# Kernel tuning notes

Hardware: AMD Instinct MI355X
Metric: run time of the kernel (lower is better)

The kernel has to match this reference:

```python
import jax, jax.numpy as jnp
import numpy as np
import math

NFFT = 2048; HOP = 512; BINS = NFFT // 2 + 1  # 1025
HEADS = 2; D = 2 * BINS; DFF = 4 * D          # 2050, 8200
BATCH = 4; LEN = 441000


def _stft(x, window):
    # replicates torch.stft(center=True, pad_mode='reflect', onesided=True)
    pad = NFFT // 2
    xp = jnp.pad(x, ((0, 0), (pad, pad)), mode='reflect')
    n_frames = 1 + (xp.shape[-1] - NFFT) // HOP
    idx = jnp.arange(n_frames)[:, None] * HOP + jnp.arange(NFFT)[None, :]
    frames = xp[:, idx] * window                      # (N, T, NFFT)
    return jnp.fft.rfft(frames, axis=-1).transpose(0, 2, 1)  # (N, BINS, T)


def _istft(spec, window, length):
    # replicates torch.istft(center=True, length=length)
    frames = jnp.fft.irfft(spec.transpose(0, 2, 1), n=NFFT, axis=-1) * window  # (N,T,NFFT)
    T = frames.shape[1]
    out_len = NFFT + HOP * (T - 1)
    idx = jnp.arange(T)[:, None] * HOP + jnp.arange(NFFT)[None, :]
    out = jnp.zeros((frames.shape[0], out_len), frames.dtype).at[:, idx].add(frames)
    wsq = jnp.zeros((out_len,), window.dtype).at[idx].add(window ** 2)
    out = out / jnp.where(wsq > 1e-11, wsq, 1.0)
    pad = NFFT // 2
    return out[:, pad:pad + length]


def _pos_enc(d, T):
    pos = jnp.arange(T, dtype=jnp.float32)[:, None]
    div = jnp.exp(jnp.arange(0, d, 2, dtype=jnp.float32) * (-math.log(10000.0) / d))
    pe = jnp.zeros((T, d), jnp.float32)
    pe = pe.at[:, 0::2].set(jnp.sin(pos * div)).at[:, 1::2].set(jnp.cos(pos * div))
    return pe[None]


def _ln(x, g, b):
    m = x.mean(-1, keepdims=True)
    v = x.var(-1, keepdims=True)
    return (x - m) / jnp.sqrt(v + 1e-5) * g + b


def _clin(r, i, Wr, br, Wi, bi):
    # (Lr(r) - Li(i), Lr(i) + Li(r))
    return (r @ Wr.T + br) - (i @ Wi.T + bi), (i @ Wr.T + br) + (r @ Wi.T + bi)


def _cconv1x1(r, i, wr, br, wi, bi):
    # 1x1 grouped conv with in=out=2, groups=2 -> per-channel scale+bias
    s = lambda x, w, b: x * w[None, :, None, None] + b[None, :, None, None]
    return s(r, wr, br) - s(i, wi, bi), s(i, wr, br) + s(r, wi, bi)


def _cattn(r, i, Win, bin_, Wo, bo):
    # 8 shared-weight MHA calls; only 4 distinct (Q,K) softmax maps, each
    # applied to two V tensors (the fusion opportunity). Eval mode: no dropout.
    B, S, _ = r.shape
    hd = D // HEADS
    Wq, Wk, Wv = Win[:D], Win[D:2 * D], Win[2 * D:]
    bq, bk, bv = bin_[:D], bin_[D:2 * D], bin_[2 * D:]
    proj = lambda x, W, b: (x @ W.T + b).reshape(B, S, HEADS, hd).transpose(0, 2, 1, 3)
    qr, qi = proj(r, Wq, bq), proj(i, Wq, bq)
    kr, ki = proj(r, Wk, bk), proj(i, Wk, bk)
    vr, vi = proj(r, Wv, bv), proj(i, Wv, bv)
    scale = 1.0 / math.sqrt(hd)
    A = lambda q, k: jax.nn.softmax(jnp.einsum('bhqd,bhkd->bhqk', q, k) * scale, axis=-1)
    Arr, Ari, Air, Aii = A(qr, kr), A(qr, ki), A(qi, kr), A(qi, ki)
    ap = lambda Aw, v: jnp.einsum('bhqk,bhkd->bhqd', Aw, v)
    out_r = ap(Arr, vr) + ap(Ari, vi) - ap(Air, vi) - ap(Aii, vr)
    out_i = ap(Arr, vi) + ap(Ari, vr) + ap(Air, vr) - ap(Aii, vi)
    merge = lambda o: o.transpose(0, 2, 1, 3).reshape(B, S, D)
    # out_proj bias coefficients: real part (+1+1-1-1)=0, imag part (+1+1+1-1)=2
    return merge(out_r) @ Wo.T, merge(out_i) @ Wo.T + 2.0 * bo


def reference(mix, window, c1wr, c1br, c1wi, c1bi, c2wr, c2br, c2wi, c2bi,
              attn_in_w, attn_in_b, attn_out_w, attn_out_b,
              l1wr, l1br, l1wi, l1bi, l2wr, l2br, l2wi, l2bi,
              n1_gr, n1_br, n1_gi, n1_bi, n2_gr, n2_br, n2_gi, n2_bi):
    B, C, L = mix.shape
    spec = _stft(mix.reshape(-1, L), window)      # (B*2, BINS, T)
    T = spec.shape[-1]
    spec = spec.reshape(-1, 2, BINS, T)           # (B, 2, BINS, T)
    real, imag = jnp.real(spec), jnp.imag(spec)
    nr, ni = _cconv1x1(real, imag, c1wr, c1br, c1wi, c1bi)
    nr = nr.transpose(0, 3, 2, 1).reshape(B, T, D)   # torch .transpose(1,3).reshape
    ni = ni.transpose(0, 3, 2, 1).reshape(B, T, D)
    pe = _pos_enc(D, T)
    nr, ni = nr + pe, ni + pe
    nr, ni = _cattn(nr, ni, attn_in_w, attn_in_b, attn_out_w, attn_out_b)
    nr, ni = _ln(nr, n1_gr, n1_br), _ln(ni, n1_gi, n1_bi)   # dropout = identity (eval)
    hr, hi = _clin(nr, ni, l1wr, l1br, l1wi, l1bi)
    hr, hi = jax.nn.relu(hr), jax.nn.relu(hi)
    hr, hi = _clin(hr, hi, l2wr, l2br, l2wi, l2bi)
    nr, ni = _ln(hr, n2_gr, n2_br), _ln(hi, n2_gi, n2_bi)
    nr = nr.reshape(B, T, BINS, 2).transpose(0, 3, 2, 1)    # (B,2,BINS,T)
    ni = ni.reshape(B, T, BINS, 2).transpose(0, 3, 2, 1)
    mr, mi = _cconv1x1(nr, ni, c2wr, c2br, c2wi, c2bi)
    real = real * jax.nn.sigmoid(mr)
    imag = imag * jax.nn.sigmoid(mi)
    spec2 = (real + 1j * imag).reshape(-1, BINS, T)
    estim = _istft(spec2, window, L).reshape(-1, 2, L)
    return estim, jnp.stack((jnp.real(spec2), jnp.imag(spec2)), axis=-1)


def setup_inputs() -> dict:
    key = jax.random.key(0)
    ks = jax.random.split(key, 32)
    W = 0.02
    rn = lambda k, shp, s=W: jax.random.normal(k, shp, jnp.float32) * s
    hann = 0.5 * (1.0 - jnp.cos(2.0 * jnp.pi * jnp.arange(NFFT, dtype=jnp.float32) / NFFT))
    inp = {
        'mix': rn(ks[0], (BATCH, 2, LEN), 1.0),
        'window': hann,
        'c1wr': rn(ks[1], (2,), 0.5), 'c1br': rn(ks[2], (2,), 0.1),
        'c1wi': rn(ks[3], (2,), 0.5), 'c1bi': rn(ks[4], (2,), 0.1),
        'c2wr': rn(ks[5], (2,), 0.5), 'c2br': rn(ks[6], (2,), 0.1),
        'c2wi': rn(ks[7], (2,), 0.5), 'c2bi': rn(ks[8], (2,), 0.1),
        'attn_in_w': rn(ks[9], (3 * D, D)), 'attn_in_b': rn(ks[10], (3 * D,)),
        'attn_out_w': rn(ks[11], (D, D)), 'attn_out_b': rn(ks[12], (D,)),
        'l1wr': rn(ks[13], (DFF, D)), 'l1br': rn(ks[14], (DFF,)),
        'l1wi': rn(ks[15], (DFF, D)), 'l1bi': rn(ks[16], (DFF,)),
        'l2wr': rn(ks[17], (D, DFF)), 'l2br': rn(ks[18], (D,)),
        'l2wi': rn(ks[19], (D, DFF)), 'l2bi': rn(ks[20], (D,)),
        'n1_gr': jnp.ones((D,), jnp.float32), 'n1_br': jnp.zeros((D,), jnp.float32),
        'n1_gi': jnp.ones((D,), jnp.float32), 'n1_bi': jnp.zeros((D,), jnp.float32),
        'n2_gr': jnp.ones((D,), jnp.float32), 'n2_br': jnp.zeros((D,), jnp.float32),
        'n2_gi': jnp.ones((D,), jnp.float32), 'n2_bi': jnp.zeros((D,), jnp.float32),
    }
    return inp
```

## Files before the change

kernel.cpp:

```cpp
#include <hip/hip_runtime.h>
#include <hip/hip_bf16.h>
#include <math.h>

#ifndef M_PIf
#define M_PIf 3.14159265358979323846f
#endif

static constexpr int kNFFT = 2048;
static constexpr int kHOP  = 512;
static constexpr int kBINS = 1025;
static constexpr int kT    = 862;
static constexpr int kL    = 441000;
static constexpr int kB    = 4;
static constexpr int kNSIG = 8;
static constexpr int kD    = 2050;
static constexpr int kHD   = 1025;
static constexpr int kDFF  = 8200;
static constexpr int kBS   = kB * kT;
static constexpr float kAttnScale = 0.031234752377721214f;
static constexpr long kS2  = (long)kT * kT;
static constexpr int kTP   = 864;
static constexpr long kS2P = (long)kT * kTP;
static constexpr int kDP   = 2056;
static constexpr int kHDP  = 1032;
static constexpr int kHDP2 = 1056;
static constexpr int kQKr  = 3488;
static constexpr int kWr   = 1152;
static constexpr int kNH   = 4104;
static constexpr int kDP2  = 2080;
static constexpr int kNHP  = 4128;
static constexpr int kMP   = 3456;
static constexpr int kW1R  = 4224;
static constexpr int kW2R  = 2176;

using bf16 = __hip_bfloat16;
typedef __attribute__((ext_vector_type(4))) float f32x4;
typedef __attribute__((ext_vector_type(8))) short bf16x8;

__device__ __forceinline__ float ldf(const float* p, long i) { return p[i]; }
__device__ __forceinline__ float ldf(const bf16* p, long i) {
  return __bfloat162float(p[i]);
}
__device__ __forceinline__ void sto(float* p, long i, float v) { p[i] = v; }
__device__ __forceinline__ void sto(bf16* p, long i, float v) {
  p[i] = __float2bfloat16(v);
}
__device__ __forceinline__ void load16(const float* src, bf16* dst) {
#pragma unroll
  for (int e = 0; e < 16; ++e) dst[e] = __float2bfloat16(src[e]);
}
__device__ __forceinline__ void load16(const bf16* src, bf16* dst) {
  *(bf16x8*)(dst)     = *(const bf16x8*)(src);
  *(bf16x8*)(dst + 8) = *(const bf16x8*)(src + 8);
}

__device__ __forceinline__ void glds16(const bf16* g, bf16* l) {
  __builtin_amdgcn_global_load_lds(
      (const __attribute__((address_space(1))) unsigned int*)g,
      (__attribute__((address_space(3))) unsigned int*)l, 16, 0, 0);
}

__device__ __forceinline__ void xcd_swizzle(int& bx, int& by) {
  int nwg = gridDim.x * gridDim.y;
  int orig = by * gridDim.x + bx;
  int qq = nwg >> 3, rr = nwg & 7;
  int xcd = orig & 7, loc = orig >> 3;
  int wg = (xcd < rr ? xcd * (qq + 1) : rr * (qq + 1) + (xcd - rr) * qq) + loc;
  bx = wg % gridDim.x;
  by = wg / gridDim.x;
}

__device__ __forceinline__ void pipe_wait8() {
  asm volatile("s_waitcnt vmcnt(8)" ::: "memory");
  __builtin_amdgcn_sched_barrier(0);
  __builtin_amdgcn_s_barrier();
  __builtin_amdgcn_sched_barrier(0);
}
__device__ __forceinline__ void pipe_wait0() {
  asm volatile("s_waitcnt vmcnt(0)" ::: "memory");
  __builtin_amdgcn_sched_barrier(0);
  __builtin_amdgcn_s_barrier();
  __builtin_amdgcn_sched_barrier(0);
}
__device__ __forceinline__ void pipe_readdone() {
  __builtin_amdgcn_sched_barrier(0);
  __builtin_amdgcn_s_barrier();
  __builtin_amdgcn_sched_barrier(0);
}

template <typename T>
__device__ __forceinline__ void stage_row16(const T* S, int grow, int glim,
                                            int lda, int k0sk, int K,
                                            bf16* dst) {
  bf16 tmp[16];
  if (grow < glim && k0sk + 16 <= K) {
    load16(S + (long)grow * lda + k0sk, tmp);
  } else {
#pragma unroll
    for (int e = 0; e < 16; ++e) {
      int gk = k0sk + e;
      tmp[e] = __float2bfloat16(
          (grow < glim && gk < K) ? ldf(S, (long)grow * lda + gk) : 0.f);
    }
  }
  *(bf16x8*)(dst)     = *(bf16x8*)&tmp[0];
  *(bf16x8*)(dst + 8) = *(bf16x8*)&tmp[8];
}

__global__ void k_twiddle(float2* __restrict__ tw) {
  int m = blockIdx.x * 256 + threadIdx.x;
  if (m < 1024) {
    float s, c;
    sincosf(M_PIf * (float)m / 1024.f, &s, &c);
    tw[m] = make_float2(c, s);
  }
}

__device__ __forceinline__ void fft2048_lds(float*& sr, float*& si,
                                            float* dr, float* di, int tid,
                                            float dir,
                                            const float2* __restrict__ tw) {
  int s = 0;
  for (int Ns = 1; Ns < 2048; Ns <<= 1, ++s) {
#pragma unroll
    for (int q = 0; q < 4; ++q) {
      int j = tid + q * 256;
      int base = j & (Ns - 1);
      int grp = j >> s;
      float2 t = tw[base << (10 - s)];
      float c = t.x, sn = dir * t.y;
      float ar = sr[j],        ai = si[j];
      float br = sr[j + 1024], bi = si[j + 1024];
      float tbr = br * c - bi * sn;
      float tbi = br * sn + bi * c;
      int o = (grp << (s + 1)) + base;
      dr[o]      = ar + tbr;  di[o]      = ai + tbi;
      dr[o + Ns] = ar - tbr;  di[o + Ns] = ai - tbi;
    }
    __syncthreads();
    float* t0 = sr; sr = dr; dr = t0;
    float* t1 = si; si = di; di = t1;
  }
}

__global__ __launch_bounds__(256) void k_stft(const float* __restrict__ mix,
                                              const float* __restrict__ win,
                                              const float2* __restrict__ tw,
                                              float* __restrict__ spec) {
  __shared__ float b0r[2048], b0i[2048], b1r[2048], b1i[2048];
  int t = blockIdx.x, sig = blockIdx.y, tid = threadIdx.x;
  const float* x = mix + (long)sig * kL;
  for (int i = tid; i < 2048; i += 256) {
    int src = t * kHOP + i - 1024;
    if (src < 0) src = -src;
    if (src >= kL) src = 2 * kL - 2 - src;
    b0r[i] = x[src] * win[i];
    b0i[i] = 0.f;
  }
  __syncthreads();
  float* sr = b0r; float* si = b0i;
  fft2048_lds(sr, si, b1r, b1i, tid, -1.f, tw);
  for (int k = tid; k < kBINS; k += 256) {
    long o = ((long)sig * kBINS + k) * kT + t;
    spec[o * 2]     = sr[k];
    spec[o * 2 + 1] = si[k];
  }
}

__global__ __launch_bounds__(256) void k_istft(const float* __restrict__ spec,
                                               const float* __restrict__ win,
                                               const float2* __restrict__ tw,
                                               float* __restrict__ frames) {
  __shared__ float b0r[2048], b0i[2048], b1r[2048], b1i[2048];
  int t = blockIdx.x, sig = blockIdx.y, tid = threadIdx.x;
  for (int k = tid; k < kBINS; k += 256) {
    long o = ((long)sig * kBINS + k) * kT + t;
    b0r[k] = spec[o * 2];
    b0i[k] = spec[o * 2 + 1];
  }
  __syncthreads();
  for (int k = 1025 + tid; k < 2048; k += 256) {
    b0r[k] = b0r[2048 - k];
    b0i[k] = -b0i[2048 - k];
  }
  __syncthreads();
  float* sr = b0r; float* si = b0i;
  fft2048_lds(sr, si, b1r, b1i, tid, +1.f, tw);
  const float scale = 1.f / 2048.f;
  float* fo = frames + ((long)sig * kT + t) * 2048;
  for (int n = tid; n < 2048; n += 256) fo[n] = sr[n] * scale * win[n];
}

__global__ void k_gather(const float* __restrict__ frames,
                         const float* __restrict__ win,
                         float* __restrict__ out0) {
  long idx = (long)blockIdx.x * 256 + threadIdx.x;
  long total = (long)kNSIG * kL;
  if (idx >= total) return;
  int sig = (int)(idx / kL);
  int l = (int)(idx % kL);
  int j = l + 1024;
  int tmax = j >> 9; if (tmax > kT - 1) tmax = kT - 1;
  int v = j - 1536;
  int tmin = v > 0 ? (v >> 9) : 0;
  float acc = 0.f, w2 = 0.f;
  for (int t = tmin; t <= tmax; ++t) {
    int n = j - (t << 9);
    float w = win[n];
    acc += frames[((long)sig * kT + t) * 2048 + n];
    w2 = fmaf(w, w, w2);
  }
  out0[idx] = acc / (w2 > 1e-11f ? w2 : 1.f);
}

__global__ void k_conv1_pe(const float* __restrict__ spec,
                           const float* __restrict__ c1wr, const float* __restrict__ c1br,
                           const float* __restrict__ c1wi, const float* __restrict__ c1bi,
                           bf16* __restrict__ xrh, bf16* __restrict__ xrl,
                           bf16* __restrict__ xih, bf16* __restrict__ xil) {
  long idx = (long)blockIdx.x * 256 + threadIdx.x;
  long total = (long)kB * 2 * kBINS * kT;
  if (idx >= total) return;
  int t = (int)(idx % kT);
  long r0 = idx / kT;
  int bin = (int)(r0 % kBINS);
  long r1 = r0 / kBINS;
  int ch = (int)(r1 % 2);
  int b = (int)(r1 / 2);
  float re = spec[idx * 2], im = spec[idx * 2 + 1];
  float wr = c1wr[ch], br = c1br[ch], wi = c1wi[ch], bi = c1bi[ch];
  float nr = (re * wr + br) - (im * wi + bi);
  float ni = (im * wr + br) + (re * wi + bi);
  int d = bin * 2 + ch;
  int k = d >> 1;
  float dv = expf((float)k * (-9.210340371976184f / 1025.0f));
  float arg = (float)t * dv;
  float pe = (d & 1) ? cosf(arg) : sinf(arg);
  long ro = ((long)(b * kT + t)) * kDP2 + d;
  float vr = nr + pe, vi = ni + pe;
  bf16 hr = __float2bfloat16(vr);
  bf16 hi = __float2bfloat16(vi);
  xrh[ro] = hr; xrl[ro] = __float2bfloat16(vr - __bfloat162float(hr));
  xih[ro] = hi; xil[ro] = __float2bfloat16(vi - __bfloat162float(hi));
}

__global__ void k_cvt2(const float* __restrict__ src, bf16* __restrict__ dst,
                       long total, int ldd, int srows, int scols, int lds) {
  long idx = (long)blockIdx.x * 256 + threadIdx.x;
  if (idx >= total) return;
  int r = (int)(idx / ldd), c = (int)(idx % ldd);
  float v = (r < srows && c < scols) ? src[(long)r * lds + c] : 0.f;
  dst[idx] = __float2bfloat16(v);
}

__global__ void k_cvt2s(const float* __restrict__ src, bf16* __restrict__ dh,
                        bf16* __restrict__ dl, long total, int ldd, int srows,
                        int scols, int lds) {
  long idx = (long)blockIdx.x * 256 + threadIdx.x;
  if (idx >= total) return;
  int r = (int)(idx / ldd), c = (int)(idx % ldd);
  float v = (r < srows && c < scols) ? src[(long)r * lds + c] : 0.f;
  bf16 h = __float2bfloat16(v);
  dh[idx] = h;
  dl[idx] = __float2bfloat16(v - __bfloat162float(h));
}

template <typename TA, typename TC>
__global__ __launch_bounds__(256) void k_mfma2(
    const TA* __restrict__ A1, const TA* __restrict__ A2,
    const bf16* __restrict__ B, TC* __restrict__ C1, TC* __restrict__ C2,
    const float* __restrict__ bias, float bs1, float bs2,
    int M, int N, int K, int lda, int ldb, int ldc) {
  __shared__ __align__(16) bf16 As1[128][40];
  __shared__ __align__(16) bf16 As2[128][40];
  __shared__ __align__(16) bf16 Bs[128][40];
  int tid = threadIdx.x;
  int bm = blockIdx.y * 128, bn = blockIdx.x * 128;
  int lane = tid & 63, w = tid >> 6;
  int wr = (w >> 1) * 64, wc = (w & 1) * 64;
  int fr = lane & 15, fq = lane >> 4;
  f32x4 ac1[4][4] = {}, ac2[4][4] = {};
  int sr = tid >> 1, sk = (tid & 1) * 16;
  for (int k0 = 0; k0 < K; k0 += 32) {
    stage_row16(A1, bm + sr, M, lda, k0 + sk, K, &As1[sr][sk]);
    stage_row16(A2, bm + sr, M, lda, k0 + sk, K, &As2[sr][sk]);
    stage_row16(B,  bn + sr, N, ldb, k0 + sk, K, &Bs[sr][sk]);
    __syncthreads();
    bf16x8 a1[4], a2[4], b[4];
#pragma unroll
    for (int i = 0; i < 4; ++i) {
      a1[i] = *(const bf16x8*)&As1[wr + i * 16 + fr][fq * 8];
      a2[i] = *(const bf16x8*)&As2[wr + i * 16 + fr][fq * 8];
      b[i]  = *(const bf16x8*)&Bs[wc + i * 16 + fr][fq * 8];
    }
#pragma unroll
    for (int i = 0; i < 4; ++i)
#pragma unroll
      for (int j = 0; j < 4; ++j) {
        ac1[i][j] = __builtin_amdgcn_mfma_f32_16x16x32_bf16(a1[i], b[j], ac1[i][j], 0, 0, 0);
        ac2[i][j] = __builtin_amdgcn_mfma_f32_16x16x32_bf16(a2[i], b[j], ac2[i][j], 0, 0, 0);
      }
    __syncthreads();
  }
#pragma unroll
  for (int i = 0; i < 4; ++i)
#pragma unroll
    for (int j = 0; j < 4; ++j) {
      int gn = bn + wc + j * 16 + fr;
      if (gn >= N) continue;
      float bv = bias ? bias[gn] : 0.f;
#pragma unroll
      for (int r = 0; r < 4; ++r) {
        int gm = bm + wr + i * 16 + fq * 4 + r;
        if (gm >= M) continue;
        long co = (long)gm * ldc + gn;
        sto(C1, co, ac1[i][j][r] + bs1 * bv);
        sto(C2, co, ac2[i][j][r] + bs2 * bv);
      }
    }
}

__global__ __launch_bounds__(256) void k_gemm3s(
    const bf16* __restrict__ Ah, const bf16* __restrict__ Al,
    const bf16* __restrict__ Bh, const bf16* __restrict__ Bl,
    bf16* __restrict__ Ch, bf16* __restrict__ Cl,
    const float* __restrict__ bias,
    int M, int N, int K, int lda, int ldb, int ldc) {
  __shared__ __align__(16) bf16 Sah[2][128][32];
  __shared__ __align__(16) bf16 Sal[2][128][32];
  __shared__ __align__(16) bf16 Sbh[2][128][32];
  __shared__ __align__(16) bf16 Sbl[2][128][32];
  int bx = blockIdx.x, by = blockIdx.y;
  xcd_swizzle(bx, by);
  int bm = by * 128, bn = bx * 128;
  int tid = threadIdx.x;
  int lane = tid & 63, w = tid >> 6;
  int wr = (w >> 1) * 64, wc = (w & 1) * 64;
  int fr = lane & 15, fq = lane >> 4;
  f32x4 acc[4][4] = {};
  int srow = w * 32 + (lane >> 2);
  int scol = (lane & 3) * 8;
  const bf16* pAh[2]; const bf16* pAl[2];
  const bf16* pBh[2]; const bf16* pBl[2];
#pragma unroll
  for (int c = 0; c < 2; ++c) {
    long ga = (long)(bm + srow + c * 16) * lda + scol;
    long gb = (long)(bn + srow + c * 16) * ldb + scol;
    pAh[c] = Ah + ga; pAl[c] = Al + ga;
    pBh[c] = Bh + gb; pBl[c] = Bl + gb;
  }
  int nt = K >> 5;
#pragma unroll
  for (int c = 0; c < 2; ++c) {
    int lb = w * 1024 + c * 512;
    glds16(pAh[c], &Sah[0][0][0] + lb);
    glds16(pAl[c], &Sal[0][0][0] + lb);
    glds16(pBh[c], &Sbh[0][0][0] + lb);
    glds16(pBl[c], &Sbl[0][0][0] + lb);
  }
  if (nt > 1) {
#pragma unroll
    for (int c = 0; c < 2; ++c) {
      int lb = 4096 + w * 1024 + c * 512;
      glds16(pAh[c] + 32, &Sah[0][0][0] + lb);
      glds16(pAl[c] + 32, &Sal[0][0][0] + lb);
      glds16(pBh[c] + 32, &Sbh[0][0][0] + lb);
      glds16(pBl[c] + 32, &Sbl[0][0][0] + lb);
    }
  }
  long koff = 64;
  for (int t = 0; t < nt; ++t) {
    int p = t & 1;
    if (t + 1 < nt) pipe_wait8(); else pipe_wait0();
    bf16x8 ah[4], al[4], bh[4], bl[4];
#pragma unroll
    for (int i = 0; i < 4; ++i) {
      ah[i] = *(const bf16x8*)&Sah[p][wr + i * 16 + fr][fq * 8];
      al[i] = *(const bf16x8*)&Sal[p][wr + i * 16 + fr][fq * 8];
      bh[i] = *(const bf16x8*)&Sbh[p][wc + i * 16 + fr][fq * 8];
      bl[i] = *(const bf16x8*)&Sbl[p][wc + i * 16 + fr][fq * 8];
    }
#pragma unroll
    for (int i = 0; i < 4; ++i)
#pragma unroll
      for (int j = 0; j < 4; ++j) {
        acc[i][j] = __builtin_amdgcn_mfma_f32_16x16x32_bf16(ah[i], bh[j], acc[i][j], 0, 0, 0);
        acc[i][j] = __builtin_amdgcn_mfma_f32_16x16x32_bf16(ah[i], bl[j], acc[i][j], 0, 0, 0);
        acc[i][j] = __builtin_amdgcn_mfma_f32_16x16x32_bf16(al[i], bh[j], acc[i][j], 0, 0, 0);
      }
    pipe_readdone();
    if (t + 2 < nt) {
      int pb = p * 4096;
#pragma unroll
      for (int c = 0; c < 2; ++c) {
        int lb = pb + w * 1024 + c * 512;
        glds16(pAh[c] + koff, &Sah[0][0][0] + lb);
        glds16(pAl[c] + koff, &Sal[0][0][0] + lb);
        glds16(pBh[c] + koff, &Sbh[0][0][0] + lb);
        glds16(pBl[c] + koff, &Sbl[0][0][0] + lb);
      }
      koff += 32;
    }
  }
#pragma unroll
  for (int i = 0; i < 4; ++i)
#pragma unroll
    for (int j = 0; j < 4; ++j) {
      int gn = bn + wc + j * 16 + fr;
      if (gn >= N) continue;
      float bv = bias[gn];
#pragma unroll
      for (int r = 0; r < 4; ++r) {
        int gm = bm + wr + i * 16 + fq * 4 + r;
        if (gm >= M) continue;
        long co = (long)gm * ldc + gn;
        float v = acc[i][j][r] + bv;
        bf16 h = __float2bfloat16(v);
        Ch[co] = h;
        Cl[co] = __float2bfloat16(v - __bfloat162float(h));
      }
    }
}

__global__ __launch_bounds__(256) void k_qkt3(
    const bf16* __restrict__ Qrh, const bf16* __restrict__ Qrl,
    const bf16* __restrict__ Qih, const bf16* __restrict__ Qil,
    const bf16* __restrict__ Krh, const bf16* __restrict__ Krl,
    const bf16* __restrict__ Kih, const bf16* __restrict__ Kil,
    float* __restrict__ S, int bp) {
  __shared__ __align__(16) bf16 Sqh[2][128][32];
  __shared__ __align__(16) bf16 Sql[2][128][32];
  __shared__ __align__(16) bf16 Skh[2][128][32];
  __shared__ __align__(16) bf16 Skl[2][128][32];
  int bl = blockIdx.z >> 2, c = blockIdx.z & 3;
  int b = bp * 2 + bl;
  long roff = (long)b * kT * kHDP2;
  const bf16* qh = ((c >> 1) ? Qih : Qrh) + roff;
  const bf16* ql = ((c >> 1) ? Qil : Qrl) + roff;
  const bf16* kh = ((c & 1) ? Kih : Krh) + roff;
  const bf16* kl = ((c & 1) ? Kil : Krl) + roff;
  float* So = S + ((long)bl * 4 + c) * kS2;
  int bx = blockIdx.x, by = blockIdx.y;
  xcd_swizzle(bx, by);
  int bm = by * 128, bn = bx * 128;
  int tid = threadIdx.x;
  int lane = tid & 63, w = tid >> 6;
  int wr = (w >> 1) * 64, wc = (w & 1) * 64;
  int fr = lane & 15, fq = lane >> 4;
  f32x4 acc[4][4] = {};
  int srow = w * 32 + (lane >> 2);
  int scol = (lane & 3) * 8;
  const bf16* pQh[2]; const bf16* pQl[2];
  const bf16* pKh[2]; const bf16* pKl[2];
#pragma unroll
  for (int cc = 0; cc < 2; ++cc) {
    long ga = (long)(bm + srow + cc * 16) * kHDP2 + scol;
    long gb = (long)(bn + srow + cc * 16) * kHDP2 + scol;
    pQh[cc] = qh + ga; pQl[cc] = ql + ga;
    pKh[cc] = kh + gb; pKl[cc] = kl + gb;
  }
  int nt = kHDP2 >> 5;
#pragma unroll
  for (int cc = 0; cc < 2; ++cc) {
    int lb = w * 1024 + cc * 512;
    glds16(pQh[cc], &Sqh[0][0][0] + lb);
    glds16(pQl[cc], &Sql[0][0][0] + lb);
    glds16(pKh[cc], &Skh[0][0][0] + lb);
    glds16(pKl[cc], &Skl[0][0][0] + lb);
  }
  if (nt > 1) {
#pragma unroll
    for (int cc = 0; cc < 2; ++cc) {
      int lb = 4096 + w * 1024 + cc * 512;
      glds16(pQh[cc] + 32, &Sqh[0][0][0] + lb);
      glds16(pQl[cc] + 32, &Sql[0][0][0] + lb);
      glds16(pKh[cc] + 32, &Skh[0][0][0] + lb);
      glds16(pKl[cc] + 32, &Skl[0][0][0] + lb);
    }
  }
  long koff = 64;
  for (int t = 0; t < nt; ++t) {
    int p = t & 1;
    if (t + 1 < nt) pipe_wait8(); else pipe_wait0();
    bf16x8 ah[4], al[4], bh[4], blv[4];
#pragma unroll
    for (int i = 0; i < 4; ++i) {
      ah[i]  = *(const bf16x8*)&Sqh[p][wr + i * 16 + fr][fq * 8];
      al[i]  = *(const bf16x8*)&Sql[p][wr + i * 16 + fr][fq * 8];
      bh[i]  = *(const bf16x8*)&Skh[p][wc + i * 16 + fr][fq * 8];
      blv[i] = *(const bf16x8*)&Skl[p][wc + i * 16 + fr][fq * 8];
    }
#pragma unroll
    for (int i = 0; i < 4; ++i)
#pragma unroll
      for (int j = 0; j < 4; ++j) {
        acc[i][j] = __builtin_amdgcn_mfma_f32_16x16x32_bf16(ah[i], bh[j],  acc[i][j], 0, 0, 0);
        acc[i][j] = __builtin_amdgcn_mfma_f32_16x16x32_bf16(ah[i], blv[j], acc[i][j], 0, 0, 0);
        acc[i][j] = __builtin_amdgcn_mfma_f32_16x16x32_bf16(al[i], bh[j],  acc[i][j], 0, 0, 0);
      }
    pipe_readdone();
    if (t + 2 < nt) {
      int pb = p * 4096;
#pragma unroll
      for (int cc = 0; cc < 2; ++cc) {
        int lb = pb + w * 1024 + cc * 512;
        glds16(pQh[cc] + koff, &Sqh[0][0][0] + lb);
        glds16(pQl[cc] + koff, &Sql[0][0][0] + lb);
        glds16(pKh[cc] + koff, &Skh[0][0][0] + lb);
        glds16(pKl[cc] + koff, &Skl[0][0][0] + lb);
      }
      koff += 32;
    }
  }
#pragma unroll
  for (int i = 0; i < 4; ++i)
#pragma unroll
    for (int j = 0; j < 4; ++j) {
      int gn = bn + wc + j * 16 + fr;
      if (gn >= kT) continue;
#pragma unroll
      for (int r = 0; r < 4; ++r) {
        int gm = bm + wr + i * 16 + fq * 4 + r;
        if (gm >= kT) continue;
        So[(long)gm * kT + gn] = acc[i][j][r];
      }
    }
}

template <typename TC>
__global__ __launch_bounds__(256) void k_cgemm(
    const bf16* __restrict__ Ar, const bf16* __restrict__ Ai,
    const bf16* __restrict__ Br, const bf16* __restrict__ Bi,
    TC* __restrict__ Cr, TC* __restrict__ Ci,
    const float* __restrict__ biasR, const float* __restrict__ biasI,
    float bscale, int accum, int relu, int Nreal,
    int M, int N, int K, int lda, int ldb, int ldc) {
  __shared__ __align__(16) bf16 Asr[2][128][32];
  __shared__ __align__(16) bf16 Asi[2][128][32];
  __shared__ __align__(16) bf16 Bsr[2][128][32];
  __shared__ __align__(16) bf16 Bsi[2][128][32];
  int bx = blockIdx.x, by = blockIdx.y;
  xcd_swizzle(bx, by);
  int bm = by * 128, bn = bx * 128;
  int tid = threadIdx.x;
  int lane = tid & 63, w = tid >> 6;
  int wr = (w >> 1) * 64, wc = (w & 1) * 64;
  int fr = lane & 15, fq = lane >> 4;
  f32x4 acR[4][4] = {}, acI[4][4] = {};
  int srow = w * 32 + (lane >> 2);
  int scol = (lane & 3) * 8;
  const bf16* pA[2][2];
  const bf16* pB[2][2];
#pragma unroll
  for (int c = 0; c < 2; ++c) {
    long ga = (long)(bm + srow + c * 16) * lda + scol;
    long gb = (long)(bn + srow + c * 16) * ldb + scol;
    pA[0][c] = Ar + ga; pA[1][c] = Ai + ga;
    pB[0][c] = Br + gb; pB[1][c] = Bi + gb;
  }
  int nt = K >> 5;
#pragma unroll
  for (int c = 0; c < 2; ++c) {
    int lb = w * 1024 + c * 512;
    glds16(pA[0][c], &Asr[0][0][0] + lb);
    glds16(pA[1][c], &Asi[0][0][0] + lb);
    glds16(pB[0][c], &Bsr[0][0][0] + lb);
    glds16(pB[1][c], &Bsi[0][0][0] + lb);
  }
  if (nt > 1) {
#pragma unroll
    for (int c = 0; c < 2; ++c) {
      int lb = 4096 + w * 1024 + c * 512;
      glds16(pA[0][c] + 32, &Asr[0][0][0] + lb);
      glds16(pA[1][c] + 32, &Asi[0][0][0] + lb);
      glds16(pB[0][c] + 32, &Bsr[0][0][0] + lb);
      glds16(pB[1][c] + 32, &Bsi[0][0][0] + lb);
    }
  }
  const short ks = (short)0x8000;
  const bf16x8 sgn = {ks, ks, ks, ks, ks, ks, ks, ks};
  long koff = 64;
  for (int t = 0; t < nt; ++t) {
    int p = t & 1;
    if (t + 1 < nt) pipe_wait8(); else pipe_wait0();
    bf16x8 ar[4], ai[4], nai[4], br[4], bi[4];
#pragma unroll
    for (int i = 0; i < 4; ++i) {
      ar[i] = *(const bf16x8*)&Asr[p][wr + i * 16 + fr][fq * 8];
      ai[i] = *(const bf16x8*)&Asi[p][wr + i * 16 + fr][fq * 8];
      nai[i] = ai[i] ^ sgn;
      br[i] = *(const bf16x8*)&Bsr[p][wc + i * 16 + fr][fq * 8];
      bi[i] = *(const bf16x8*)&Bsi[p][wc + i * 16 + fr][fq * 8];
    }
#pragma unroll
    for (int i = 0; i < 4; ++i)
#pragma unroll
      for (int j = 0; j < 4; ++j) {
        acR[i][j] = __builtin_amdgcn_mfma_f32_16x16x32_bf16(ar[i],  br[j], acR[i][j], 0, 0, 0);
        acR[i][j] = __builtin_amdgcn_mfma_f32_16x16x32_bf16(nai[i], bi[j], acR[i][j], 0, 0, 0);
        acI[i][j] = __builtin_amdgcn_mfma_f32_16x16x32_bf16(ai[i],  br[j], acI[i][j], 0, 0, 0);
        acI[i][j] = __builtin_amdgcn_mfma_f32_16x16x32_bf16(ar[i],  bi[j], acI[i][j], 0, 0, 0);
      }
    pipe_readdone();
    if (t + 2 < nt) {
      int pb = p * 4096;
#pragma unroll
      for (int c = 0; c < 2; ++c) {
        int lb = pb + w * 1024 + c * 512;
        glds16(pA[0][c] + koff, &Asr[0][0][0] + lb);
        glds16(pA[1][c] + koff, &Asi[0][0][0] + lb);
        glds16(pB[0][c] + koff, &Bsr[0][0][0] + lb);
        glds16(pB[1][c] + koff, &Bsi[0][0][0] + lb);
      }
      koff += 32;
    }
  }
#pragma unroll
  for (int i = 0; i < 4; ++i)
#pragma unroll
    for (int j = 0; j < 4; ++j) {
      int gn = bn + wc + j * 16 + fr;
      if (gn >= N) continue;
      float br_ = 0.f, bi_ = 0.f;
      if (gn < Nreal) { br_ = biasR[gn]; bi_ = biasI[gn]; }
#pragma unroll
      for (int r = 0; r < 4; ++r) {
        int gm = bm + wr + i * 16 + fq * 4 + r;
        if (gm >= M) continue;
        long co = (long)gm * ldc + gn;
        float vR = acR[i][j][r] + bscale * (br_ - bi_);
        float vI = acI[i][j][r] + bscale * (br_ + bi_);
        if (accum) { vR += ldf(Cr, co); vI += ldf(Ci, co); }
        if (relu) { vR = fmaxf(vR, 0.f); vI = fmaxf(vI, 0.f); }
        sto(Cr, co, vR);
        sto(Ci, co, vI);
      }
    }
}

__global__ __launch_bounds__(256) void k_pv(
    const bf16* __restrict__ P, const bf16* __restrict__ Vr,
    const bf16* __restrict__ Vi, bf16* __restrict__ Cr,
    bf16* __restrict__ Ci, int M, int N, int K, int ldp, int ldv, int ldc) {
  __shared__ __align__(16) bf16 Ps0[128][40];
  __shared__ __align__(16) bf16 Ps1[128][40];
  __shared__ __align__(16) bf16 Ps2[128][40];
  __shared__ __align__(16) bf16 Vsr[128][40];
  __shared__ __align__(16) bf16 Vsi[128][40];
  int tid = threadIdx.x;
  int bm = blockIdx.y * 128, bn = blockIdx.x * 128;
  int lane = tid & 63, w = tid >> 6;
  int wr = (w >> 1) * 64, wc = (w & 1) * 64;
  int fr = lane & 15, fq = lane >> 4;
  f32x4 acR[4][4] = {}, acI[4][4] = {};
  int sr = tid >> 1, sk = (tid & 1) * 16;
  int kk = tid >> 3, nq = (tid & 7) * 16;
  for (int k0 = 0; k0 < K; k0 += 32) {
    stage_row16(P,            bm + sr, M, ldp, k0 + sk, K, &Ps0[sr][sk]);
    stage_row16(P + kS2P,     bm + sr, M, ldp, k0 + sk, K, &Ps1[sr][sk]);
    stage_row16(P + 2 * kS2P, bm + sr, M, ldp, k0 + sk, K, &Ps2[sr][sk]);
    {
      int gk = k0 + kk;
      bf16 t0[16], t1[16];
      if (gk < K && bn + nq + 16 <= N) {
        load16(Vr + (long)gk * ldv + bn + nq, t0);
        load16(Vi + (long)gk * ldv + bn + nq, t1);
      } else {
#pragma unroll
        for (int e = 0; e < 16; ++e) {
          int gn = bn + nq + e;
          bool ok = (gk < K && gn < N);
          t0[e] = __float2bfloat16(ok ? ldf(Vr, (long)gk * ldv + gn) : 0.f);
          t1[e] = __float2bfloat16(ok ? ldf(Vi, (long)gk * ldv + gn) : 0.f);
        }
      }
#pragma unroll
      for (int e = 0; e < 16; ++e) {
        Vsr[nq + e][kk] = t0[e];
        Vsi[nq + e][kk] = t1[e];
      }
    }
    __syncthreads();
    bf16x8 p0[4], p1[4], p2[4], vr[4], vi[4];
#pragma unroll
    for (int i = 0; i < 4; ++i) {
      p0[i] = *(const bf16x8*)&Ps0[wr + i * 16 + fr][fq * 8];
      p1[i] = *(const bf16x8*)&Ps1[wr + i * 16 + fr][fq * 8];
      p2[i] = *(const bf16x8*)&Ps2[wr + i * 16 + fr][fq * 8];
      vr[i] = *(const bf16x8*)&Vsr[wc + i * 16 + fr][fq * 8];
      vi[i] = *(const bf16x8*)&Vsi[wc + i * 16 + fr][fq * 8];
    }
#pragma unroll
    for (int i = 0; i < 4; ++i)
#pragma unroll
      for (int j = 0; j < 4; ++j) {
        acR[i][j] = __builtin_amdgcn_mfma_f32_16x16x32_bf16(p0[i], vr[j], acR[i][j], 0, 0, 0);
        acR[i][j] = __builtin_amdgcn_mfma_f32_16x16x32_bf16(p2[i], vi[j], acR[i][j], 0, 0, 0);
        acI[i][j] = __builtin_amdgcn_mfma_f32_16x16x32_bf16(p0[i], vi[j], acI[i][j], 0, 0, 0);
        acI[i][j] = __builtin_amdgcn_mfma_f32_16x16x32_bf16(p1[i], vr[j], acI[i][j], 0, 0, 0);
      }
    __syncthreads();
  }
#pragma unroll
  for (int i = 0; i < 4; ++i)
#pragma unroll
    for (int j = 0; j < 4; ++j) {
      int gn = bn + wc + j * 16 + fr;
      if (gn >= N) continue;
#pragma unroll
      for (int r = 0; r < 4; ++r) {
        int gm = bm + wr + i * 16 + fq * 4 + r;
        if (gm >= M) continue;
        long co = (long)gm * ldc + gn;
        Cr[co] = __float2bfloat16(acR[i][j][r]);
        Ci[co] = __float2bfloat16(acI[i][j][r]);
      }
    }
}

__global__ __launch_bounds__(256) void k_smf(const float* __restrict__ S,
                                             bf16* __restrict__ P) {
  long rbase = (long)blockIdx.x * kT;
  long pbase = (long)blockIdx.x * kTP;
  int tid = threadIdx.x;
  int lane = tid & 63, w = tid >> 6;
  float v[4][4];
  float mx[4] = {-3.4e38f, -3.4e38f, -3.4e38f, -3.4e38f};
#pragma unroll
  for (int c = 0; c < 4; ++c) {
    const float* row = S + c * kS2 + rbase;
#pragma unroll
    for (int q = 0; q < 4; ++q) {
      int i = tid + q * 256;
      v[c][q] = (i < kT) ? row[i] : -3.4e38f;
      mx[c] = fmaxf(mx[c], v[c][q]);
    }
  }
  __shared__ float redm[4][4];
  for (int o = 32; o > 0; o >>= 1)
#pragma unroll
    for (int c = 0; c < 4; ++c) mx[c] = fmaxf(mx[c], __shfl_down(mx[c], o));
  if (lane == 0)
#pragma unroll
    for (int c = 0; c < 4; ++c) redm[w][c] = mx[c];
  __syncthreads();
#pragma unroll
  for (int c = 0; c < 4; ++c)
    mx[c] = fmaxf(fmaxf(redm[0][c], redm[1][c]), fmaxf(redm[2][c], redm[3][c]));
  __syncthreads();
  float sm[4] = {0.f, 0.f, 0.f, 0.f};
#pragma unroll
  for (int c = 0; c < 4; ++c)
#pragma unroll
    for (int q = 0; q < 4; ++q) {
      int i = tid + q * 256;
      if (i < kT) {
        v[c][q] = expf(kAttnScale * (v[c][q] - mx[c]));
        sm[c] += v[c][q];
      }
    }
  __shared__ float reds[4][4];
  for (int o = 32; o > 0; o >>= 1)
#pragma unroll
    for (int c = 0; c < 4; ++c) sm[c] += __shfl_down(sm[c], o);
  if (lane == 0)
#pragma unroll
    for (int c = 0; c < 4; ++c) reds[w][c] = sm[c];
  __syncthreads();
  float inv[4];
#pragma unroll
  for (int c = 0; c < 4; ++c)
    inv[c] = 1.f / (reds[0][c] + reds[1][c] + reds[2][c] + reds[3][c]);
  bf16* p0 = P + pbase;
  bf16* p1 = P + kS2P + pbase;
  bf16* p2 = P + 2 * kS2P + pbase;
#pragma unroll
  for (int q = 0; q < 4; ++q) {
    int i = tid + q * 256;
    if (i >= kT) continue;
    float a0 = v[0][q] * inv[0], a1 = v[1][q] * inv[1];
    float a2 = v[2][q] * inv[2], a3 = v[3][q] * inv[3];
    p0[i] = __float2bfloat16(a0 - a3);
    p1[i] = __float2bfloat16(a1 + a2);
    p2[i] = __float2bfloat16(a1 - a2);
  }
}

__global__ __launch_bounds__(256) void k_ln(float* __restrict__ X,
                                            const float* __restrict__ g,
                                            const float* __restrict__ b, int d) {
  long row = blockIdx.x;
  float* x = X + row * d;
  int tid = threadIdx.x;
  float s = 0.f, s2 = 0.f;
  for (int i = tid; i < d; i += 256) {
    float v = x[i];
    s += v;
    s2 = fmaf(v, v, s2);
  }
  __shared__ float rs[4], rs2[4];
  for (int o = 32; o > 0; o >>= 1) {
    s += __shfl_down(s, o);
    s2 += __shfl_down(s2, o);
  }
  int lane = tid & 63, w = tid >> 6;
  if (lane == 0) { rs[w] = s; rs2[w] = s2; }
  __syncthreads();
  float st = rs[0] + rs[1] + rs[2] + rs[3];
  float s2t = rs2[0] + rs2[1] + rs2[2] + rs2[3];
  float m = st / d;
  float var = s2t / d - m * m;
  float inv = rsqrtf(var + 1e-5f);
  for (int i = tid; i < d; i += 256) x[i] = (x[i] - m) * inv * g[i] + b[i];
}

__global__ void k_mask(const float* __restrict__ gr_, const float* __restrict__ gi_,
                       const float* __restrict__ c2wr, const float* __restrict__ c2br,
                       const float* __restrict__ c2wi, const float* __restrict__ c2bi,
                       float* __restrict__ spec) {
  long idx = (long)blockIdx.x * 256 + threadIdx.x;
  long total = (long)kB * 2 * kBINS * kT;
  if (idx >= total) return;
  int t = (int)(idx % kT);
  long r0 = idx / kT;
  int bin = (int)(r0 % kBINS);
  long r1 = r0 / kBINS;
  int ch = (int)(r1 % 2);
  int b = (int)(r1 / 2);
  long ro = ((long)(b * kT + t)) * kD + (bin * 2 + ch);
  float gr = gr_[ro], gi = gi_[ro];
  float wr = c2wr[ch], br = c2br[ch], wi = c2wi[ch], bi = c2bi[ch];
  float mr = (gr * wr + br) - (gi * wi + bi);
  float mi = (gi * wr + br) + (gr * wi + bi);
  float re = spec[idx * 2], im = spec[idx * 2 + 1];
  spec[idx * 2]     = re / (1.f + expf(-mr));
  spec[idx * 2 + 1] = im / (1.f + expf(-mi));
}

extern "C" void kernel_launch(void* const* d_in, const int* in_sizes, int n_in,
                              void* d_out, int out_size, void* d_ws, size_t ws_size,
                              hipStream_t stream) {
  const float* mix        = (const float*)d_in[0];
  const float* window     = (const float*)d_in[1];
  const float* c1wr       = (const float*)d_in[2];
  const float* c1br       = (const float*)d_in[3];
  const float* c1wi       = (const float*)d_in[4];
  const float* c1bi       = (const float*)d_in[5];
  const float* c2wr       = (const float*)d_in[6];
  const float* c2br       = (const float*)d_in[7];
  const float* c2wi       = (const float*)d_in[8];
  const float* c2bi       = (const float*)d_in[9];
  const float* attn_in_w  = (const float*)d_in[10];
  const float* attn_in_b  = (const float*)d_in[11];
  const float* attn_out_w = (const float*)d_in[12];
  const float* attn_out_b = (const float*)d_in[13];
  const float* l1wr       = (const float*)d_in[14];
  const float* l1br       = (const float*)d_in[15];
  const float* l1wi       = (const float*)d_in[16];
  const float* l1bi       = (const float*)d_in[17];
  const float* l2wr       = (const float*)d_in[18];
  const float* l2br       = (const float*)d_in[19];
  const float* l2wi       = (const float*)d_in[20];
  const float* l2bi       = (const float*)d_in[21];
  const float* n1_gr      = (const float*)d_in[22];
  const float* n1_br      = (const float*)d_in[23];
  const float* n1_gi      = (const float*)d_in[24];
  const float* n1_bi      = (const float*)d_in[25];
  const float* n2_gr      = (const float*)d_in[26];
  const float* n2_br      = (const float*)d_in[27];
  const float* n2_gi      = (const float*)d_in[28];
  const float* n2_bi      = (const float*)d_in[29];

  constexpr long eX    = (long)kMP * kDP2;
  constexpr long eQK2  = (long)kQKr * kHDP2;
  constexpr long eAout = (long)kBS * kDP;
  constexpr long eV    = (long)kBS * kHDP;
  constexpr long eWp   = (long)kWr * kDP2;
  constexpr long eHidp = (long)kMP * kNHP;
  constexpr long eW1p  = (long)kW1R * kDP2;
  constexpr long eW2p  = (long)kW2R * kNHP;

  constexpr size_t oX    = 0;
  constexpr size_t oQK   = oX + 4 * eX * 2;
  constexpr size_t oAout = oQK + 8 * eQK2 * 2;
  constexpr size_t oV    = oAout + 2 * eAout * 2;
  constexpr size_t oW    = oV + 2 * eV * 2;
  constexpr size_t oP    = oW + 5 * eWp * 2;
  constexpr size_t oTW   = oP + 3 * kS2P * 2;
  constexpr size_t kNeed = 188922816;
  static_assert(oTW + 8192 <= kNeed, "tw overflow");
  constexpr size_t oSS = oW;
  static_assert(oSS + 8 * kS2 * 4 <= oP, "sS overflow");
  static_assert(2 * (long)kBS * kD * 4 <= (long)oQK, "xr/xi overlay");
  static_assert((long)kD * kDP * 2 <= (long)(oW - oV), "Wob overlay");
  constexpr size_t oAb  = oQK;
  constexpr size_t oWF  = oAb + 2 * eX * 2;
  constexpr size_t oHid = oWF + 2 * eW2p * 2;
  static_assert(2 * eW1p * 2 <= 2 * eW2p * 2, "W slot sized by W2");
  static_assert(oHid + 2 * eHidp * 2 <= oTW, "hid overflow");
  static_assert((long)kNSIG * kT * 2048 * 4 <= (long)(oTW - oAb), "frames");

  char* wsb = (char*)d_ws;
  if (ws_size < kNeed) return;

  bf16*  Xrh = (bf16*)(wsb + oX);
  bf16*  Xrl = Xrh + eX;
  bf16*  Xih = Xrl + eX;
  bf16*  Xil = Xih + eX;
  bf16*  Qrh = (bf16*)(wsb + oQK);
  bf16*  Qrl = Qrh + eQK2;
  bf16*  Qih = Qrl + eQK2;
  bf16*  Qil = Qih + eQK2;
  bf16*  Krh = Qil + eQK2;
  bf16*  Krl = Krh + eQK2;
  bf16*  Kih = Krl + eQK2;
  bf16*  Kil = Kih + eQK2;
  bf16*  aoutR = (bf16*)(wsb + oAout);
  bf16*  aoutI = aoutR + eAout;
  bf16*  Vr = (bf16*)(wsb + oV);
  bf16*  Vi = Vr + eV;
  bf16*  Wqh = (bf16*)(wsb + oW);
  bf16*  Wql = Wqh + eWp;
  bf16*  Wkh = Wql + eWp;
  bf16*  Wkl = Wkh + eWp;
  bf16*  Wvh = Wkl + eWp;
  float* sS = (float*)(wsb + oSS);
  bf16*  Pbuf = (bf16*)(wsb + oP);
  bf16*  Wob = (bf16*)(wsb + oV);
  float* xr = (float*)(wsb + oX);
  float* xi = xr + (long)kBS * kD;
  bf16*  AbR = (bf16*)(wsb + oAb);
  bf16*  AbI = AbR + eX;
  bf16*  w1rH = (bf16*)(wsb + oWF);
  bf16*  w1iH = w1rH + eW1p;
  bf16*  w2rH = (bf16*)(wsb + oWF);
  bf16*  w2iH = w2rH + eW2p;
  bf16*  hidR = (bf16*)(wsb + oHid);
  bf16*  hidI = hidR + eHidp;
  float* frames = (float*)(wsb + oAb);
  float2* tw = (float2*)(wsb + oTW);

  float* out0 = (float*)d_out;
  float* spec = out0 + (long)kNSIG * kL;

  auto cvt2 = [&](const float* src, bf16* dst, int dstRows, int ldd,
                  int srows, int scols, int lds) {
    long total = (long)dstRows * ldd;
    k_cvt2<<<(int)((total + 255) / 256), 256, 0, stream>>>(src, dst, total,
                                                           ldd, srows, scols,
                                                           lds);
  };
  auto cvt2s = [&](const float* src, bf16* dh, bf16* dl, int dstRows, int ldd,
                   int srows, int scols, int lds) {
    long total = (long)dstRows * ldd;
    k_cvt2s<<<(int)((total + 255) / 256), 256, 0, stream>>>(
        src, dh, dl, total, ldd, srows, scols, lds);
  };

  hipMemsetAsync(d_ws, 0, kNeed, stream);
  k_twiddle<<<4, 256, 0, stream>>>(tw);

  k_stft<<<dim3(kT, kNSIG), 256, 0, stream>>>(mix, window, tw, spec);

  long nct = (long)kB * 2 * kBINS * kT;
  k_conv1_pe<<<(nct + 255) / 256, 256, 0, stream>>>(spec, c1wr, c1br, c1wi,
                                                    c1bi, Xrh, Xrl, Xih, Xil);

  for (int h = 0; h < 2; ++h) {
    const float* Wq = attn_in_w + (long)(h * kHD) * kD;
    const float* Wk = attn_in_w + (long)(kD + h * kHD) * kD;
    const float* Wv = attn_in_w + (long)(2 * kD + h * kHD) * kD;
    const float* bq = attn_in_b + h * kHD;
    const float* bk = attn_in_b + kD + h * kHD;
    const float* bv = attn_in_b + 2 * kD + h * kHD;
    cvt2s(Wq, Wqh, Wql, kWr, kDP2, kHD, kD, kD);
    cvt2s(Wk, Wkh, Wkl, kWr, kDP2, kHD, kD, kD);
    cvt2(Wv, Wvh, kWr, kDP2, kHD, kD, kD);
    k_mfma2<bf16, bf16><<<dim3(9, 27), 256, 0, stream>>>(
        Xrh, Xih, Wvh, Vr, Vi, bv, 1.f, 1.f, kBS, kHD, kD, kDP2, kDP2, kHDP);
    k_gemm3s<<<dim3(9, 27), 256, 0, stream>>>(
        Xrh, Xrl, Wqh, Wql, Qrh, Qrl, bq, kBS, kHD, kDP2, kDP2, kDP2, kHDP2);
    k_gemm3s<<<dim3(9, 27), 256, 0, stream>>>(
        Xih, Xil, Wqh, Wql, Qih, Qil, bq, kBS, kHD, kDP2, kDP2, kDP2, kHDP2);
    k_gemm3s<<<dim3(9, 27), 256, 0, stream>>>(
        Xrh, Xrl, Wkh, Wkl, Krh, Krl, bk, kBS, kHD, kDP2, kDP2, kDP2, kHDP2);
    k_gemm3s<<<dim3(9, 27), 256, 0, stream>>>(
        Xih, Xil, Wkh, Wkl, Kih, Kil, bk, kBS, kHD, kDP2, kDP2, kDP2, kHDP2);
    for (int bp = 0; bp < 2; ++bp) {
      k_qkt3<<<dim3(7, 7, 8), 256, 0, stream>>>(Qrh, Qrl, Qih, Qil,
                                                Krh, Krl, Kih, Kil, sS, bp);
      for (int bl = 0; bl < 2; ++bl) {
        int b = bp * 2 + bl;
        k_smf<<<kT, 256, 0, stream>>>(sS + (long)bl * 4 * kS2, Pbuf);
        k_pv<<<dim3(9, 7), 256, 0, stream>>>(
            Pbuf, Vr + (long)b * kT * kHDP, Vi + (long)b * kT * kHDP,
            aoutR + (long)b * kT * kDP + h * kHD,
            aoutI + (long)b * kT * kDP + h * kHD,
            kT, kHD, kT, kTP, kHDP, kDP);
      }
    }
  }

  cvt2(attn_out_w, Wob, kD, kDP, kD, kD, kD);
  k_mfma2<bf16, float><<<dim3(17, 27), 256, 0, stream>>>(
      aoutR, aoutI, Wob, xr, xi, attn_out_b, 0.f, 2.f,
      kBS, kD, kD, kDP, kDP, kD);

  k_ln<<<kBS, 256, 0, stream>>>(xr, n1_gr, n1_br, kD);
  k_ln<<<kBS, 256, 0, stream>>>(xi, n1_gi, n1_bi, kD);

  cvt2(xr, AbR, kMP, kDP2, kBS, kD, kD);
  cvt2(xi, AbI, kMP, kDP2, kBS, kD, kD);
  for (int nh = 0; nh < 2; ++nh) {
    int srows = (nh ? kDFF - kNH : kNH);
    cvt2(l1wr + (long)nh * kNH * kD, w1rH, kW1R, kDP2, srows, kD, kD);
    cvt2(l1wi + (long)nh * kNH * kD, w1iH, kW1R, kDP2, srows, kD, kD);
    k_cgemm<bf16><<<dim3(33, 27), 256, 0, stream>>>(
        AbR, AbI, w1rH, w1iH, hidR, hidI,
        l1br + nh * kNH, l1bi + nh * kNH, 1.f, 0, 1, srows,
        kBS, kNHP, kDP2, kDP2, kDP2, kNHP);
    cvt2(l2wr + nh * kNH, w2rH, kW2R, kNHP, kD, srows, kDFF);
    cvt2(l2wi + nh * kNH, w2iH, kW2R, kNHP, kD, srows, kDFF);
    k_cgemm<float><<<dim3(17, 27), 256, 0, stream>>>(
        hidR, hidI, w2rH, w2iH, xr, xi,
        l2br, l2bi, (nh == 0 ? 1.f : 0.f), nh, 0, kD,
        kBS, kD, kNHP, kNHP, kNHP, kD);
  }

  k_ln<<<kBS, 256, 0, stream>>>(xr, n2_gr, n2_br, kD);
  k_ln<<<kBS, 256, 0, stream>>>(xi, n2_gi, n2_bi, kD);

  k_mask<<<(nct + 255) / 256, 256, 0, stream>>>(xr, xi, c2wr, c2br, c2wi,
                                                c2bi, spec);

  k_istft<<<dim3(kT, kNSIG), 256, 0, stream>>>(spec, window, tw, frames);
  k_gather<<<(int)(((long)kNSIG * kL + 255) / 256), 256, 0, stream>>>(
      frames, window, out0);
}
```

Baseline: 5.492 ms.

## Widen complex GEMM tile to 128x256 with 512 threads, drop double buffering

The complex GEMM tile grows from 128x128 to 128x256 and runs eight waves per block, so each A tile loaded into LDS is reused across twice as many output columns. In exchange, the double-buffered async-load pipeline with partial waits is replaced by a single buffer guarded by two __syncthreads per K step. Global loads therefore no longer overlap MFMA work. Weight padding buffers are enlarged so the wider tile never reads out of bounds, and the launch grids are halved in x.

```diff
diff --git a/kernel.cpp b/kernel.cpp
--- a/kernel.cpp
+++ b/kernel.cpp
@@ -30,8 +30,8 @@
 static constexpr int kDP2  = 2080;
 static constexpr int kNHP  = 4128;
 static constexpr int kMP   = 3456;
-static constexpr int kW1R  = 4224;
-static constexpr int kW2R  = 2176;
+static constexpr int kW1R  = 4352;
+static constexpr int kW2R  = 2304;
 
 using bf16 = __hip_bfloat16;
 typedef __attribute__((ext_vector_type(4))) float f32x4;
@@ -528,92 +528,69 @@
 }
 
 template <typename TC>
-__global__ __launch_bounds__(256) void k_cgemm(
+__global__ __launch_bounds__(512) void k_cgemm(
     const bf16* __restrict__ Ar, const bf16* __restrict__ Ai,
     const bf16* __restrict__ Br, const bf16* __restrict__ Bi,
     TC* __restrict__ Cr, TC* __restrict__ Ci,
     const float* __restrict__ biasR, const float* __restrict__ biasI,
     float bscale, int accum, int relu, int Nreal,
     int M, int N, int K, int lda, int ldb, int ldc) {
-  __shared__ __align__(16) bf16 Asr[2][128][32];
-  __shared__ __align__(16) bf16 Asi[2][128][32];
-  __shared__ __align__(16) bf16 Bsr[2][128][32];
-  __shared__ __align__(16) bf16 Bsi[2][128][32];
+  __shared__ __align__(16) bf16 Asr[128][32];
+  __shared__ __align__(16) bf16 Asi[128][32];
+  __shared__ __align__(16) bf16 Bsr[256][32];
+  __shared__ __align__(16) bf16 Bsi[256][32];
   int bx = blockIdx.x, by = blockIdx.y;
   xcd_swizzle(bx, by);
-  int bm = by * 128, bn = bx * 128;
+  int bm = by * 128, bn = bx * 256;
   int tid = threadIdx.x;
   int lane = tid & 63, w = tid >> 6;
-  int wr = (w >> 1) * 64, wc = (w & 1) * 64;
+  int wr = (w >> 2) * 64, wc = (w & 3) * 64;
   int fr = lane & 15, fq = lane >> 4;
   f32x4 acR[4][4] = {}, acI[4][4] = {};
-  int srow = w * 32 + (lane >> 2);
+  int srow = w * 16 + (lane >> 2);
   int scol = (lane & 3) * 8;
-  const bf16* pA[2][2];
-  const bf16* pB[2][2];
+  const bf16* pAr = Ar + (long)(bm + srow) * lda + scol;
+  const bf16* pAi = Ai + (long)(bm + srow) * lda + scol;
+  const bf16* pBr[2];
+  const bf16* pBi[2];
 #pragma unroll
   for (int c = 0; c < 2; ++c) {
-    long ga = (long)(bm + srow + c * 16) * lda + scol;
-    long gb = (long)(bn + srow + c * 16) * ldb + scol;
-    pA[0][c] = Ar + ga; pA[1][c] = Ai + ga;
-    pB[0][c] = Br + gb; pB[1][c] = Bi + gb;
-  }
-  int nt = K >> 5;
-#pragma unroll
-  for (int c = 0; c < 2; ++c) {
-    int lb = w * 1024 + c * 512;
-    glds16(pA[0][c], &Asr[0][0][0] + lb);
-    glds16(pA[1][c], &Asi[0][0][0] + lb);
-    glds16(pB[0][c], &Bsr[0][0][0] + lb);
-    glds16(pB[1][c], &Bsi[0][0][0] + lb);
-  }
-  if (nt > 1) {
-#pragma unroll
-    for (int c = 0; c < 2; ++c) {
-      int lb = 4096 + w * 1024 + c * 512;
-      glds16(pA[0][c] + 32, &Asr[0][0][0] + lb);
-      glds16(pA[1][c] + 32, &Asi[0][0][0] + lb);
-      glds16(pB[0][c] + 32, &Bsr[0][0][0] + lb);
-      glds16(pB[1][c] + 32, &Bsi[0][0][0] + lb);
-    }
+    long gb = (long)(bn + c * 128 + srow) * ldb + scol;
+    pBr[c] = Br + gb;
+    pBi[c] = Bi + gb;
   }
   const short ks = (short)0x8000;
   const bf16x8 sgn = {ks, ks, ks, ks, ks, ks, ks, ks};
-  long koff = 64;
-  for (int t = 0; t < nt; ++t) {
-    int p = t & 1;
-    if (t + 1 < nt) pipe_wait8(); else pipe_wait0();
-    bf16x8 ar[4], ai[4], nai[4], br[4], bi[4];
+  for (int k0 = 0; k0 < K; k0 += 32) {
+    glds16(pAr + k0, &Asr[0][0] + w * 512);
+    glds16(pAi + k0, &Asi[0][0] + w * 512);
+#pragma unroll
+    for (int c = 0; c < 2; ++c) {
+      int lb = c * 4096 + w * 512;
+      glds16(pBr[c] + k0, &Bsr[0][0] + lb);
+      glds16(pBi[c] + k0, &Bsi[0][0] + lb);
+    }
+    __syncthreads();
+    bf16x8 ar[4], ai[4], nai[4];
 #pragma unroll
     for (int i = 0; i < 4; ++i) {
-      ar[i] = *(const bf16x8*)&Asr[p][wr + i * 16 + fr][fq * 8];
-      ai[i] = *(const bf16x8*)&Asi[p][wr + i * 16 + fr][fq * 8];
+      ar[i] = *(const bf16x8*)&Asr[wr + i * 16 + fr][fq * 8];
+      ai[i] = *(const bf16x8*)&Asi[wr + i * 16 + fr][fq * 8];
       nai[i] = ai[i] ^ sgn;
-      br[i] = *(const bf16x8*)&Bsr[p][wc + i * 16 + fr][fq * 8];
-      bi[i] = *(const bf16x8*)&Bsi[p][wc + i * 16 + fr][fq * 8];
-    }
-#pragma unroll
-    for (int i = 0; i < 4; ++i)
-#pragma unroll
-      for (int j = 0; j < 4; ++j) {
-        acR[i][j] = __builtin_amdgcn_mfma_f32_16x16x32_bf16(ar[i],  br[j], acR[i][j], 0, 0, 0);
-        acR[i][j] = __builtin_amdgcn_mfma_f32_16x16x32_bf16(nai[i], bi[j], acR[i][j], 0, 0, 0);
-        acI[i][j] = __builtin_amdgcn_mfma_f32_16x16x32_bf16(ai[i],  br[j], acI[i][j], 0, 0, 0);
-        acI[i][j] = __builtin_amdgcn_mfma_f32_16x16x32_bf16(ar[i],  bi[j], acI[i][j], 0, 0, 0);
-      }
-    pipe_readdone();
-    if (t + 2 < nt) {
-      int pb = p * 4096;
-#pragma unroll
-      for (int c = 0; c < 2; ++c) {
-        int lb = pb + w * 1024 + c * 512;
-        glds16(pA[0][c] + koff, &Asr[0][0][0] + lb);
-        glds16(pA[1][c] + koff, &Asi[0][0][0] + lb);
-        glds16(pB[0][c] + koff, &Bsr[0][0][0] + lb);
-        glds16(pB[1][c] + koff, &Bsi[0][0][0] + lb);
-      }
-      koff += 32;
-    }
+    }
+#pragma unroll
+    for (int j = 0; j < 4; ++j) {
+      bf16x8 br = *(const bf16x8*)&Bsr[wc + j * 16 + fr][fq * 8];
+      bf16x8 bi = *(const bf16x8*)&Bsi[wc + j * 16 + fr][fq * 8];
+#pragma unroll
+      for (int i = 0; i < 4; ++i) {
+        acR[i][j] = __builtin_amdgcn_mfma_f32_16x16x32_bf16(ar[i],  br, acR[i][j], 0, 0, 0);
+        acR[i][j] = __builtin_amdgcn_mfma_f32_16x16x32_bf16(nai[i], bi, acR[i][j], 0, 0, 0);
+        acI[i][j] = __builtin_amdgcn_mfma_f32_16x16x32_bf16(ai[i],  br, acI[i][j], 0, 0, 0);
+        acI[i][j] = __builtin_amdgcn_mfma_f32_16x16x32_bf16(ar[i],  bi, acI[i][j], 0, 0, 0);
+      }
+    }
+    __syncthreads();
   }
 #pragma unroll
   for (int i = 0; i < 4; ++i)
@@ -1015,13 +992,13 @@
     int srows = (nh ? kDFF - kNH : kNH);
     cvt2(l1wr + (long)nh * kNH * kD, w1rH, kW1R, kDP2, srows, kD, kD);
     cvt2(l1wi + (long)nh * kNH * kD, w1iH, kW1R, kDP2, srows, kD, kD);
-    k_cgemm<bf16><<<dim3(33, 27), 256, 0, stream>>>(
+    k_cgemm<bf16><<<dim3(17, 27), 512, 0, stream>>>(
         AbR, AbI, w1rH, w1iH, hidR, hidI,
         l1br + nh * kNH, l1bi + nh * kNH, 1.f, 0, 1, srows,
         kBS, kNHP, kDP2, kDP2, kDP2, kNHP);
     cvt2(l2wr + nh * kNH, w2rH, kW2R, kNHP, kD, srows, kDFF);
     cvt2(l2wi + nh * kNH, w2iH, kW2R, kNHP, kD, srows, kDFF);
-    k_cgemm<float><<<dim3(17, 27), 256, 0, stream>>>(
+    k_cgemm<float><<<dim3(9, 27), 512, 0, stream>>>(
         hidR, hidI, w2rH, w2iH, xr, xi,
         l2br, l2bi, (nh == 0 ? 1.f : 0.f), nh, 0, kD,
         kBS, kD, kNHP, kNHP, kNHP, kD);
```

Measured after the change: 4.941 ms. 1.11x faster.
